# Performance work log

Hardware: AMD Instinct MI355X
Metric: run time of the kernel (lower is better)

## Reference

```python
import jax, jax.numpy as jnp
import numpy as np

K = 16        # neighbors
TAU = 0.1     # softmax temperature
BETA = 1.0    # knn loss weight
LAMB = 1e-4   # l2 reg weight
EPS = 1e-8    # clamp floor


def setup_inputs() -> dict:
    key = jax.random.key(0)
    k1, k2, k3, k4, k5, k6 = jax.random.split(key, 6)
    B, d, N, NQ = 256, 128, 100000, 4096
    q_batch = jax.random.normal(k1, (B, d), dtype=jnp.float32)
    q_indices = jax.random.randint(k2, (B,), 0, NQ, dtype=jnp.int64)
    X = jax.random.normal(k3, (N, d), dtype=jnp.float32)
    W = jax.random.normal(k4, (d, d), dtype=jnp.float32) * (1.0 / np.sqrt(d))
    pre_indices = jax.random.randint(k5, (NQ, K), 0, N, dtype=jnp.int64)
    pw = jax.random.uniform(k6, (NQ, K), dtype=jnp.float32) + 0.05
    pre_weights = pw / pw.sum(axis=1, keepdims=True)  # precomputed softmax weights
    return {"q_batch": q_batch, "q_indices": q_indices, "X": X, "W": W,
            "pre_indices": pre_indices, "pre_weights": pre_weights}


def reference(q_batch, q_indices, X, W, pre_indices, pre_weights):
    B = q_batch.shape[0]
    N = X.shape[0]
    # model(q_batch): linear map
    T_q = q_batch @ W  # [B, d]
    # brute-force faiss search: exact L2 top-K (indices are non-differentiable,
    # matching the detached faiss search in the original).
    Tq_sg = jax.lax.stop_gradient(T_q)
    d2 = (jnp.sum(Tq_sg * Tq_sg, axis=1, keepdims=True)
          + jnp.sum(X * X, axis=1)[None, :]
          - 2.0 * Tq_sg @ X.T)  # [B, N]
    _, post_idx = jax.lax.top_k(-d2, K)  # [B, K] nearest neighbors
    # recompute exact squared distances with gradient through T_q
    X_nb = X[post_idx]  # [B, K, d]
    l2 = jnp.sum((T_q[:, None, :] - X_nb) ** 2, axis=-1)  # [B, K]
    post_w = jax.nn.softmax(-l2 / TAU, axis=1)  # [B, K]
    # per-sample precomputed distributions
    pre_idx_b = pre_indices[q_indices]  # [B, K]
    pre_w_b = pre_weights[q_indices]    # [B, K]
    # dense scatter over the database axis (vectorized union construction)
    rows = jnp.arange(B)[:, None]
    p_dense = jnp.zeros((B, N), jnp.float32).at[rows, pre_idx_b].set(pre_w_b)
    q_dense = jnp.zeros((B, N), jnp.float32).at[rows, post_idx].set(post_w)
    union = (p_dense > 0) | (q_dense > 0)  # [B, N] union-of-indices mask
    p = jnp.where(union, jnp.maximum(p_dense, EPS), 0.0)
    p = p / p.sum(axis=1, keepdims=True)
    q = jnp.where(union, jnp.maximum(q_dense, EPS), 0.0)
    q = q / q.sum(axis=1, keepdims=True)
    # KL(p || q) summed over the union, averaged over batch
    logp = jnp.where(union, jnp.log(jnp.maximum(p, 1e-20)), 0.0)
    logq = jnp.where(union, jnp.log(jnp.maximum(q, 1e-20)), 0.0)
    kl = jnp.sum(jnp.where(union, p * (logp - logq), 0.0), axis=1)  # [B]
    loss_knn = jnp.mean(kl)
    loss_reg = 0.5 * jnp.sum(W * W)
    loss_dist = jnp.float32(0.0)
    total_loss = BETA * loss_knn + LAMB * loss_reg
    return (total_loss, loss_dist, loss_knn)
```

## Files before the change

### kernel.cpp

```cpp
#include <hip/hip_runtime.h>
#include <math.h>

#define KNN 16
#define DIM 128
#define BQ 256
#define NDB 100000
#define GRID 512
#define RPP 32
#define NCHUNK 3125
#define LONGB 53
#define XB_STR 136
#define MREG 8
#define CAPS 256
#define TAU_INV 10.0f
#define EPSC 1e-8f
#define FBIG 3.402823e38f

typedef float f32x4 __attribute__((ext_vector_type(4)));
typedef __bf16 bf16x8 __attribute__((ext_vector_type(8)));
typedef unsigned short ushort;
typedef ushort ushort8 __attribute__((ext_vector_type(8)));
typedef unsigned int uint4v __attribute__((ext_vector_type(4)));

__device__ __forceinline__ ushort f32_to_bf16_rne(float v) {
    unsigned bits = __float_as_uint(v);
    return (ushort)((bits + 0x7FFFu + ((bits >> 16) & 1u)) >> 16);
}
__device__ __forceinline__ unsigned pack2(float lo, float hi) {
    return (__float_as_uint(hi) & 0xFFFF0000u) | (__float_as_uint(lo) >> 16);
}
__device__ __forceinline__ float packv(float v, int id) {
    return __uint_as_float((__float_as_uint(v) & 0xFFFFFF00u) | (unsigned)id);
}

__global__ void k_tq(const float* __restrict__ qb, const float* __restrict__ W,
                     float* __restrict__ Tq, ushort* __restrict__ Tqb) {
    int b = blockIdx.x, c = threadIdx.x;
    __shared__ float qs[DIM];
    qs[c] = qb[b * DIM + c];
    __syncthreads();
    float acc = 0.f;
#pragma unroll 8
    for (int k = 0; k < DIM; ++k) acc = fmaf(qs[k], W[k * DIM + c], acc);
    Tq[b * DIM + c] = acc;
    Tqb[b * DIM + c] = f32_to_bf16_rne(acc);
}

__global__ __launch_bounds__(512, 2)
void k_pass0(const ushort* __restrict__ Tqb, const float* __restrict__ X,
             float* __restrict__ cand, float* __restrict__ blkmin_t) {
    __shared__ ushort xb[2][RPP * XB_STR];
    __shared__ float xsq_lds[2][RPP];
    const int t = threadIdx.x;
    const int w = t >> 6, lane = t & 63;
    const int la = lane >> 4, lb = lane & 15;
    const int sr = t >> 4, sc = t & 15;
    const int bid = blockIdx.x;
    const int nph = (bid < LONGB) ? 7 : 6;

    bf16x8 afr[2][4];
#pragma unroll
    for (int mt = 0; mt < 2; ++mt)
#pragma unroll
        for (int ks = 0; ks < 4; ++ks)
            afr[mt][ks] = *reinterpret_cast<const bf16x8*>(
                Tqb + (size_t)(w * 32 + mt * 16 + lb) * DIM + ks * 32 + la * 8);

    {
        const int rbase = bid * RPP;
        const float4* src = reinterpret_cast<const float4*>(X + (size_t)(rbase + sr) * DIM + sc * 8);
        float4 v0 = src[0], v1 = src[1];
        uint4v o = { pack2(v0.x, v0.y), pack2(v0.z, v0.w),
                     pack2(v1.x, v1.y), pack2(v1.z, v1.w) };
        *reinterpret_cast<uint4v*>(&xb[0][sr * XB_STR + sc * 8]) = o;
        float s = v0.x*v0.x + v0.y*v0.y + v0.z*v0.z + v0.w*v0.w
                + v1.x*v1.x + v1.y*v1.y + v1.z*v1.z + v1.w*v1.w;
        s += __shfl_xor(s, 1, 16); s += __shfl_xor(s, 2, 16);
        s += __shfl_xor(s, 4, 16); s += __shfl_xor(s, 8, 16);
        if (sc == 0) xsq_lds[0][sr] = s;
    }
    asm volatile("s_waitcnt lgkmcnt(0)" ::: "memory");
    __builtin_amdgcn_s_barrier();

    float t2_0[2][4], t2_1[2][4];
#pragma unroll
    for (int mt = 0; mt < 2; ++mt)
#pragma unroll
        for (int r = 0; r < 4; ++r) { t2_0[mt][r] = FBIG; t2_1[mt][r] = FBIG; }

#pragma unroll 1
    for (int p = 0; p < nph; ++p) {
        const int cur = p & 1, nxt = cur ^ 1;
        const int rb2 = (bid + ((p + 1) << 9)) << 5;
        float4 q0, q1;
        if (p + 1 < nph) {
            const float4* s2 = reinterpret_cast<const float4*>(X + (size_t)(rb2 + sr) * DIM + sc * 8);
            q0 = s2[0]; q1 = s2[1];
        }
#pragma unroll
        for (int nt = 0; nt < 2; ++nt) {
            const int row = nt * 16 + lb;
            bf16x8 bfr[4];
#pragma unroll
            for (int ks = 0; ks < 4; ++ks)
                bfr[ks] = *reinterpret_cast<const bf16x8*>(
                    &xb[cur][row * XB_STR + ks * 32 + la * 8]);
            const float xs = xsq_lds[cur][row];
            const int id = (((p << 1) | nt) << 4) | lb;
#pragma unroll
            for (int mt = 0; mt < 2; ++mt) {
                f32x4 acc = {0.f, 0.f, 0.f, 0.f};
#pragma unroll
                for (int ks = 0; ks < 4; ++ks)
                    acc = __builtin_amdgcn_mfma_f32_16x16x32_bf16(afr[mt][ks], bfr[ks], acc, 0, 0, 0);
#pragma unroll
                for (int r = 0; r < 4; ++r) {
                    float pv = packv(fmaf(-2.f, acc[r], xs), id);
                    float b0 = fminf(t2_0[mt][r], pv);
                    float hi = fmaxf(t2_0[mt][r], pv);
                    t2_1[mt][r] = fminf(t2_1[mt][r], hi);
                    t2_0[mt][r] = b0;
                }
            }
        }
        if (p + 1 < nph) {
            uint4v o = { pack2(q0.x, q0.y), pack2(q0.z, q0.w),
                         pack2(q1.x, q1.y), pack2(q1.z, q1.w) };
            *reinterpret_cast<uint4v*>(&xb[nxt][sr * XB_STR + sc * 8]) = o;
            float s = q0.x*q0.x + q0.y*q0.y + q0.z*q0.z + q0.w*q0.w
                    + q1.x*q1.x + q1.y*q1.y + q1.z*q1.z + q1.w*q1.w;
            s += __shfl_xor(s, 1, 16); s += __shfl_xor(s, 2, 16);
            s += __shfl_xor(s, 4, 16); s += __shfl_xor(s, 8, 16);
            if (sc == 0) xsq_lds[nxt][sr] = s;
            asm volatile("s_waitcnt lgkmcnt(0)" ::: "memory");
            __builtin_amdgcn_s_barrier();
        }
    }

#pragma unroll
    for (int mt = 0; mt < 2; ++mt)
#pragma unroll
        for (int r = 0; r < 4; ++r) {
            float a0 = t2_0[mt][r], a1 = t2_1[mt][r], a2 = FBIG, a3 = FBIG;
#pragma unroll
            for (int m = 1; m <= 8; m <<= 1) {
                float b0 = __shfl_xor(a0, m, 16), b1 = __shfl_xor(a1, m, 16);
                float b2 = __shfl_xor(a2, m, 16), b3 = __shfl_xor(a3, m, 16);
                float l0 = fminf(a0, b3), l1 = fminf(a1, b2);
                float l2 = fminf(a2, b1), l3 = fminf(a3, b0);
                float u;
                u = fminf(l0, l2); l2 = fmaxf(l0, l2); l0 = u;
                u = fminf(l1, l3); l3 = fmaxf(l1, l3); l1 = u;
                u = fminf(l0, l1); l1 = fmaxf(l0, l1); l0 = u;
                u = fminf(l2, l3); l3 = fmaxf(l2, l3); l2 = u;
                a0 = l0; a1 = l1; a2 = l2; a3 = l3;
            }
            if (lb == 0) {
                const int q = w * 32 + mt * 16 + la * 4 + r;
                f32x4 o4 = {a0, a1, a2, a3};
                *reinterpret_cast<f32x4*>(cand + (size_t)q * (GRID * 4) + bid * 4) = o4;
                blkmin_t[(size_t)q * GRID + bid] = a0;
            }
        }
}

__global__ __launch_bounds__(512)
void k_sel(const float* __restrict__ cand, const float* __restrict__ blkmin_t,
           const float* __restrict__ Tq, const float* __restrict__ X,
           const int* __restrict__ q_indices,
           const int* __restrict__ pre_indices,
           const float* __restrict__ pre_weights,
           float* __restrict__ klv) {
    const int q = blockIdx.x, t = threadIdx.x;
    __shared__ float tau_s;
    __shared__ int cnt_s;
    __shared__ float cv[CAPS]; __shared__ int ce[CAPS];
    __shared__ int post_idx[KNN];
    __shared__ float l2s[KNN];
    __shared__ float post_w[KNN];

    if (t == 0) cnt_s = 0;
    if (t < KNN) post_idx[t] = 0;
    if (t < 64) {
        float m[MREG];
#pragma unroll
        for (int k = 0; k < MREG; ++k)
            m[k] = blkmin_t[(size_t)q * GRID + t + (k << 6)];
        float tv = FBIG;
        for (int e = 0; e < KNN; ++e) {
            float best = m[0];
#pragma unroll
            for (int k = 1; k < MREG; ++k) best = fminf(best, m[k]);
            float b = best;
#pragma unroll
            for (int s = 1; s < 64; s <<= 1) b = fminf(b, __shfl_xor(b, s, 64));
            tv = b;
            unsigned long long has = __ballot(best == b);
            int src = (int)__builtin_ctzll(has);
            if (t == src) {
                bool dn = false;
#pragma unroll
                for (int k = 0; k < MREG; ++k) {
                    bool hit = !dn && (m[k] == b);
                    if (hit) { m[k] = FBIG; dn = true; }
                }
            }
        }
        if (t == 0) tau_s = tv;
    }
    __syncthreads();
    const float tau = tau_s;

    for (int e = t; e < GRID * 4; e += 512) {
        float pv = cand[(size_t)q * (GRID * 4) + e];
        if (pv <= tau) {
            int pos = atomicAdd(&cnt_s, 1);
            if (pos < CAPS) { cv[pos] = pv; ce[pos] = e; }
        }
    }
    __syncthreads();
    int n = cnt_s; n = (n > CAPS) ? CAPS : n;

    for (int e = t; e < n; e += 512) {
        float v = cv[e]; int id = ce[e];
        int r = 0;
        for (int i2 = 0; i2 < n; ++i2) {
            float vi = cv[i2];
            r += (vi < v) || (vi == v && ce[i2] < id);
        }
        if (r < KNN) {
            int bid = id >> 2;
            int sid = __float_as_uint(v) & 255;
            int j = (bid + (sid >> 5) * GRID) * RPP + ((sid >> 4) & 1) * 16 + (sid & 15);
            post_idx[r] = j;
        }
    }
    __syncthreads();

    if (t < 256) {
        int nn = t >> 4, l = t & 15;
        int idx = post_idx[nn];
        idx = (idx < 0) ? 0 : ((idx >= NDB) ? NDB - 1 : idx);
        const float* tr = Tq + q * DIM + l * 8;
        const float* xr = X + (size_t)idx * DIM + l * 8;
        float s = 0.f;
#pragma unroll
        for (int kk = 0; kk < 8; ++kk) { float df = tr[kk] - xr[kk]; s = fmaf(df, df, s); }
#pragma unroll
        for (int m = 1; m < 16; m <<= 1) s += __shfl_xor(s, m, 64);
        if (l == 0) l2s[nn] = s;
    }
    __syncthreads();

    if (t < 64) {
        float v = (t < KNN) ? (-l2s[t] * TAU_INV) : -FBIG;
        float mx = v;
#pragma unroll
        for (int m = 1; m < 16; m <<= 1) mx = fmaxf(mx, __shfl_xor(mx, m, 64));
        float e = (t < KNN) ? expf(v - mx) : 0.f;
        float sum = e;
#pragma unroll
        for (int m = 1; m < 16; m <<= 1) sum += __shfl_xor(sum, m, 64);
        if (t < KNN) post_w[t] = e / sum;

        int ui = (t < KNN) ? post_idx[t] : -1;
        float uq = (t < KNN) ? post_w[t] : 0.f;
        float up = 0.f;
        int cnt2 = KNN;
        const int qi = q_indices[q];
        for (int m = 0; m < KNN; ++m) {
            int pi = pre_indices[qi * KNN + m];
            float pwm = pre_weights[qi * KNN + m];
            unsigned long long mm = __ballot(ui == pi);
            if (mm) {
                if (t == (int)__builtin_ctzll(mm)) up = pwm;
            } else {
                if (t == cnt2) { ui = pi; up = pwm; uq = 0.f; }
                ++cnt2;
            }
        }
        float pe = 0.f, qe = 0.f, te = 0.f;
        if (t < cnt2) {
            pe = fmaxf(up, EPSC);
            qe = fmaxf(uq, EPSC);
            te = pe * (logf(pe) - logf(qe));
        }
        float Zp = pe, Zq = qe, T = te;
#pragma unroll
        for (int m = 1; m < 64; m <<= 1) {
            Zp += __shfl_xor(Zp, m, 64);
            Zq += __shfl_xor(Zq, m, 64);
            T  += __shfl_xor(T, m, 64);
        }
        if (t == 0) klv[q] = T / Zp - logf(Zp) + logf(Zq);
    }
}

__global__ void k_out(const float* __restrict__ kl, const float* __restrict__ W,
                      float* __restrict__ out) {
    int t = threadIdx.x;
    float s_kl = (t < BQ) ? kl[t] : 0.f;
    float s_w = 0.f;
    for (int i = t; i < DIM * DIM; i += 256) { float w = W[i]; s_w = fmaf(w, w, s_w); }
#pragma unroll
    for (int m = 32; m >= 1; m >>= 1) {
        s_kl += __shfl_xor(s_kl, m, 64);
        s_w += __shfl_xor(s_w, m, 64);
    }
    __shared__ float rk[4], rw[4];
    if ((t & 63) == 0) { rk[t >> 6] = s_kl; rw[t >> 6] = s_w; }
    __syncthreads();
    if (t == 0) {
        float kls = rk[0] + rk[1] + rk[2] + rk[3];
        float wss = rw[0] + rw[1] + rw[2] + rw[3];
        float knn = kls * (1.0f / BQ);
        float reg = 0.5f * wss;
        out[0] = 1.0f * knn + 1e-4f * reg;
        out[1] = 0.f;
        out[2] = knn;
    }
}

extern "C" void kernel_launch(void* const* d_in, const int* in_sizes, int n_in,
                              void* d_out, int out_size, void* d_ws, size_t ws_size,
                              hipStream_t stream) {
    const float* q_batch     = (const float*)d_in[0];
    const int*   q_indices   = (const int*)d_in[1];
    const float* X           = (const float*)d_in[2];
    const float* W           = (const float*)d_in[3];
    const int*   pre_indices = (const int*)d_in[4];
    const float* pre_weights = (const float*)d_in[5];

    char* ws = (char*)d_ws;
    float*  Tq      = (float*)(ws);
    ushort* Tqb     = (ushort*)(ws + 131072);
    float*  klv     = (float*)(ws + 196608);
    float*  blkmint = (float*)(ws + 262144);
    float*  cand    = (float*)(ws + 1048576);

    k_tq<<<dim3(BQ), dim3(DIM), 0, stream>>>(q_batch, W, Tq, Tqb);
    k_pass0<<<dim3(GRID), dim3(512), 0, stream>>>(Tqb, X, cand, blkmint);
    k_sel<<<dim3(BQ), dim3(512), 0, stream>>>(cand, blkmint, Tq, X,
                                              q_indices, pre_indices, pre_weights, klv);
    k_out<<<dim3(1), dim3(256), 0, stream>>>(klv, W, (float*)d_out);
}
```

Measured before the change: 63.43 us.

## Double rows per tile to 64 in the bf16 MFMA distance pass

Each block now stages 64 database rows per phase instead of 32, so there are half as many phases and barriers per block. Each thread loads 64 bytes per row chunk. Because 100000 is not a multiple of 64*512, the last chunk is padded: loads are clamped and out-of-range rows get distance FBIG. The packed candidate id encoding and its decode back to a database index are changed to match. The larger tile doubles LDS use, which may lower occupancy, and the final chunk partly wastes work.

```diff
diff --git a/kernel.cpp b/kernel.cpp
--- a/kernel.cpp
+++ b/kernel.cpp
@@ -6,9 +6,9 @@
 #define BQ 256
 #define NDB 100000
 #define GRID 512
-#define RPP 32
-#define NCHUNK 3125
-#define LONGB 53
+#define RPP 64
+#define NCHUNK 1563
+#define LONGB 27
 #define XB_STR 136
 #define MREG 8
 #define CAPS 256
@@ -19,7 +19,6 @@
 typedef float f32x4 __attribute__((ext_vector_type(4)));
 typedef __bf16 bf16x8 __attribute__((ext_vector_type(8)));
 typedef unsigned short ushort;
-typedef ushort ushort8 __attribute__((ext_vector_type(8)));
 typedef unsigned int uint4v __attribute__((ext_vector_type(4)));
 
 __device__ __forceinline__ ushort f32_to_bf16_rne(float v) {
@@ -54,9 +53,10 @@
     const int t = threadIdx.x;
     const int w = t >> 6, lane = t & 63;
     const int la = lane >> 4, lb = lane & 15;
-    const int sr = t >> 4, sc = t & 15;
+    const int sr = t >> 3;
+    const int sc = t & 7;
     const int bid = blockIdx.x;
-    const int nph = (bid < LONGB) ? 7 : 6;
+    const int nph = (bid < LONGB) ? 4 : 3;
 
     bf16x8 afr[2][4];
 #pragma unroll
@@ -67,16 +67,20 @@
                 Tqb + (size_t)(w * 32 + mt * 16 + lb) * DIM + ks * 32 + la * 8);
 
     {
-        const int rbase = bid * RPP;
-        const float4* src = reinterpret_cast<const float4*>(X + (size_t)(rbase + sr) * DIM + sc * 8);
-        float4 v0 = src[0], v1 = src[1];
-        uint4v o = { pack2(v0.x, v0.y), pack2(v0.z, v0.w),
-                     pack2(v1.x, v1.y), pack2(v1.z, v1.w) };
-        *reinterpret_cast<uint4v*>(&xb[0][sr * XB_STR + sc * 8]) = o;
+        int j = bid * RPP + sr; int jc = (j < NDB) ? j : (NDB - 1);
+        const float4* src = reinterpret_cast<const float4*>(X + (size_t)jc * DIM + sc * 16);
+        float4 v0 = src[0], v1 = src[1], v2 = src[2], v3 = src[3];
+        uint4v o0 = { pack2(v0.x, v0.y), pack2(v0.z, v0.w),
+                      pack2(v1.x, v1.y), pack2(v1.z, v1.w) };
+        uint4v o1 = { pack2(v2.x, v2.y), pack2(v2.z, v2.w),
+                      pack2(v3.x, v3.y), pack2(v3.z, v3.w) };
+        *reinterpret_cast<uint4v*>(&xb[0][sr * XB_STR + sc * 16]) = o0;
+        *reinterpret_cast<uint4v*>(&xb[0][sr * XB_STR + sc * 16 + 8]) = o1;
         float s = v0.x*v0.x + v0.y*v0.y + v0.z*v0.z + v0.w*v0.w
-                + v1.x*v1.x + v1.y*v1.y + v1.z*v1.z + v1.w*v1.w;
-        s += __shfl_xor(s, 1, 16); s += __shfl_xor(s, 2, 16);
-        s += __shfl_xor(s, 4, 16); s += __shfl_xor(s, 8, 16);
+                + v1.x*v1.x + v1.y*v1.y + v1.z*v1.z + v1.w*v1.w
+                + v2.x*v2.x + v2.y*v2.y + v2.z*v2.z + v2.w*v2.w
+                + v3.x*v3.x + v3.y*v3.y + v3.z*v3.z + v3.w*v3.w;
+        s += __shfl_xor(s, 1, 8); s += __shfl_xor(s, 2, 8); s += __shfl_xor(s, 4, 8);
         if (sc == 0) xsq_lds[0][sr] = s;
     }
     asm volatile("s_waitcnt lgkmcnt(0)" ::: "memory");
@@ -91,14 +95,16 @@
 #pragma unroll 1
     for (int p = 0; p < nph; ++p) {
         const int cur = p & 1, nxt = cur ^ 1;
-        const int rb2 = (bid + ((p + 1) << 9)) << 5;
-        float4 q0, q1;
+        const int cbase = (bid + ((p + 1) << 9)) * RPP;
+        float4 q0, q1, q2, q3;
         if (p + 1 < nph) {
-            const float4* s2 = reinterpret_cast<const float4*>(X + (size_t)(rb2 + sr) * DIM + sc * 8);
-            q0 = s2[0]; q1 = s2[1];
-        }
-#pragma unroll
-        for (int nt = 0; nt < 2; ++nt) {
+            int j = cbase + sr; int jc = (j < NDB) ? j : (NDB - 1);
+            const float4* s2 = reinterpret_cast<const float4*>(X + (size_t)jc * DIM + sc * 16);
+            q0 = s2[0]; q1 = s2[1]; q2 = s2[2]; q3 = s2[3];
+        }
+        const int rbase = (bid + (p << 9)) * RPP;
+#pragma unroll
+        for (int nt = 0; nt < 4; ++nt) {
             const int row = nt * 16 + lb;
             bf16x8 bfr[4];
 #pragma unroll
@@ -106,7 +112,9 @@
                 bfr[ks] = *reinterpret_cast<const bf16x8*>(
                     &xb[cur][row * XB_STR + ks * 32 + la * 8]);
             const float xs = xsq_lds[cur][row];
-            const int id = (((p << 1) | nt) << 4) | lb;
+            const int j = rbase + row;
+            const bool oob = (j >= NDB);
+            const int id = (((p << 2) | nt) << 4) | lb;
 #pragma unroll
             for (int mt = 0; mt < 2; ++mt) {
                 f32x4 acc = {0.f, 0.f, 0.f, 0.f};
@@ -115,7 +123,8 @@
                     acc = __builtin_amdgcn_mfma_f32_16x16x32_bf16(afr[mt][ks], bfr[ks], acc, 0, 0, 0);
 #pragma unroll
                 for (int r = 0; r < 4; ++r) {
-                    float pv = packv(fmaf(-2.f, acc[r], xs), id);
+                    float dv = oob ? FBIG : fmaf(-2.f, acc[r], xs);
+                    float pv = packv(dv, id);
                     float b0 = fminf(t2_0[mt][r], pv);
                     float hi = fmaxf(t2_0[mt][r], pv);
                     t2_1[mt][r] = fminf(t2_1[mt][r], hi);
@@ -124,13 +133,17 @@
             }
         }
         if (p + 1 < nph) {
-            uint4v o = { pack2(q0.x, q0.y), pack2(q0.z, q0.w),
-                         pack2(q1.x, q1.y), pack2(q1.z, q1.w) };
-            *reinterpret_cast<uint4v*>(&xb[nxt][sr * XB_STR + sc * 8]) = o;
+            uint4v o0 = { pack2(q0.x, q0.y), pack2(q0.z, q0.w),
+                          pack2(q1.x, q1.y), pack2(q1.z, q1.w) };
+            uint4v o1 = { pack2(q2.x, q2.y), pack2(q2.z, q2.w),
+                          pack2(q3.x, q3.y), pack2(q3.z, q3.w) };
+            *reinterpret_cast<uint4v*>(&xb[nxt][sr * XB_STR + sc * 16]) = o0;
+            *reinterpret_cast<uint4v*>(&xb[nxt][sr * XB_STR + sc * 16 + 8]) = o1;
             float s = q0.x*q0.x + q0.y*q0.y + q0.z*q0.z + q0.w*q0.w
-                    + q1.x*q1.x + q1.y*q1.y + q1.z*q1.z + q1.w*q1.w;
-            s += __shfl_xor(s, 1, 16); s += __shfl_xor(s, 2, 16);
-            s += __shfl_xor(s, 4, 16); s += __shfl_xor(s, 8, 16);
+                    + q1.x*q1.x + q1.y*q1.y + q1.z*q1.z + q1.w*q1.w
+                    + q2.x*q2.x + q2.y*q2.y + q2.z*q2.z + q2.w*q2.w
+                    + q3.x*q3.x + q3.y*q3.y + q3.z*q3.z + q3.w*q3.w;
+            s += __shfl_xor(s, 1, 8); s += __shfl_xor(s, 2, 8); s += __shfl_xor(s, 4, 8);
             if (sc == 0) xsq_lds[nxt][sr] = s;
             asm volatile("s_waitcnt lgkmcnt(0)" ::: "memory");
             __builtin_amdgcn_s_barrier();
@@ -231,7 +244,8 @@
         if (r < KNN) {
             int bid = id >> 2;
             int sid = __float_as_uint(v) & 255;
-            int j = (bid + (sid >> 5) * GRID) * RPP + ((sid >> 4) & 1) * 16 + (sid & 15);
+            int p2 = sid >> 6, nt = (sid >> 4) & 3, lb2 = sid & 15;
+            int j = (bid + (p2 << 9)) * RPP + nt * 16 + lb2;
             post_idx[r] = j;
         }
     }
```

Result: slower. 68.46 us (+7.9%).

## Deepen X prefetch to two phases and fold final reduction into atomics

Applied to the files above, without the earlier changes.

The distance pass now issues global loads for X tiles two phases ahead, holding them in registers, so each load has a full extra phase of MFMA work to cover its latency. The separate one-block output kernel is removed. The W squared-norm term is written by block 0 of the Tq kernel, and each selection block adds its scaled KL value to the output with atomics. This saves one kernel launch and its tail, at the cost of more live registers in the pass kernel and an output sum whose float rounding depends on atomic ordering.

```diff
diff --git a/kernel.cpp b/kernel.cpp
--- a/kernel.cpp
+++ b/kernel.cpp
@@ -19,7 +19,6 @@
 typedef float f32x4 __attribute__((ext_vector_type(4)));
 typedef __bf16 bf16x8 __attribute__((ext_vector_type(8)));
 typedef unsigned short ushort;
-typedef ushort ushort8 __attribute__((ext_vector_type(8)));
 typedef unsigned int uint4v __attribute__((ext_vector_type(4)));
 
 __device__ __forceinline__ ushort f32_to_bf16_rne(float v) {
@@ -34,7 +33,8 @@
 }
 
 __global__ void k_tq(const float* __restrict__ qb, const float* __restrict__ W,
-                     float* __restrict__ Tq, ushort* __restrict__ Tqb) {
+                     float* __restrict__ Tq, ushort* __restrict__ Tqb,
+                     float* __restrict__ out) {
     int b = blockIdx.x, c = threadIdx.x;
     __shared__ float qs[DIM];
     qs[c] = qb[b * DIM + c];
@@ -44,6 +44,21 @@
     for (int k = 0; k < DIM; ++k) acc = fmaf(qs[k], W[k * DIM + c], acc);
     Tq[b * DIM + c] = acc;
     Tqb[b * DIM + c] = f32_to_bf16_rne(acc);
+
+    if (b == 0) {
+        float sw = 0.f;
+        for (int i = c; i < DIM * DIM; i += 128) { float wv = W[i]; sw = fmaf(wv, wv, sw); }
+#pragma unroll
+        for (int m = 32; m >= 1; m >>= 1) sw += __shfl_xor(sw, m, 64);
+        __shared__ float rw2[2];
+        if ((c & 63) == 0) rw2[c >> 6] = sw;
+        __syncthreads();
+        if (c == 0) {
+            out[0] = 1e-4f * 0.5f * (rw2[0] + rw2[1]);
+            out[1] = 0.f;
+            out[2] = 0.f;
+        }
+    }
 }
 
 __global__ __launch_bounds__(512, 2)
@@ -66,6 +81,7 @@
             afr[mt][ks] = *reinterpret_cast<const bf16x8*>(
                 Tqb + (size_t)(w * 32 + mt * 16 + lb) * DIM + ks * 32 + la * 8);
 
+    float4 rA0, rA1;
     {
         const int rbase = bid * RPP;
         const float4* src = reinterpret_cast<const float4*>(X + (size_t)(rbase + sr) * DIM + sc * 8);
@@ -78,6 +94,11 @@
         s += __shfl_xor(s, 1, 16); s += __shfl_xor(s, 2, 16);
         s += __shfl_xor(s, 4, 16); s += __shfl_xor(s, 8, 16);
         if (sc == 0) xsq_lds[0][sr] = s;
+        if (nph > 1) {
+            const float4* s1 = reinterpret_cast<const float4*>(
+                X + (size_t)((bid + 512) * RPP + sr) * DIM + sc * 8);
+            rA0 = s1[0]; rA1 = s1[1];
+        }
     }
     asm volatile("s_waitcnt lgkmcnt(0)" ::: "memory");
     __builtin_amdgcn_s_barrier();
@@ -91,11 +112,11 @@
 #pragma unroll 1
     for (int p = 0; p < nph; ++p) {
         const int cur = p & 1, nxt = cur ^ 1;
-        const int rb2 = (bid + ((p + 1) << 9)) << 5;
-        float4 q0, q1;
-        if (p + 1 < nph) {
-            const float4* s2 = reinterpret_cast<const float4*>(X + (size_t)(rb2 + sr) * DIM + sc * 8);
-            q0 = s2[0]; q1 = s2[1];
+        float4 rB0, rB1;
+        if (p + 2 < nph) {
+            const float4* s2 = reinterpret_cast<const float4*>(
+                X + (size_t)((bid + ((p + 2) << 9)) * RPP + sr) * DIM + sc * 8);
+            rB0 = s2[0]; rB1 = s2[1];
         }
 #pragma unroll
         for (int nt = 0; nt < 2; ++nt) {
@@ -124,17 +145,18 @@
             }
         }
         if (p + 1 < nph) {
-            uint4v o = { pack2(q0.x, q0.y), pack2(q0.z, q0.w),
-                         pack2(q1.x, q1.y), pack2(q1.z, q1.w) };
+            uint4v o = { pack2(rA0.x, rA0.y), pack2(rA0.z, rA0.w),
+                         pack2(rA1.x, rA1.y), pack2(rA1.z, rA1.w) };
             *reinterpret_cast<uint4v*>(&xb[nxt][sr * XB_STR + sc * 8]) = o;
-            float s = q0.x*q0.x + q0.y*q0.y + q0.z*q0.z + q0.w*q0.w
-                    + q1.x*q1.x + q1.y*q1.y + q1.z*q1.z + q1.w*q1.w;
+            float s = rA0.x*rA0.x + rA0.y*rA0.y + rA0.z*rA0.z + rA0.w*rA0.w
+                    + rA1.x*rA1.x + rA1.y*rA1.y + rA1.z*rA1.z + rA1.w*rA1.w;
             s += __shfl_xor(s, 1, 16); s += __shfl_xor(s, 2, 16);
             s += __shfl_xor(s, 4, 16); s += __shfl_xor(s, 8, 16);
             if (sc == 0) xsq_lds[nxt][sr] = s;
             asm volatile("s_waitcnt lgkmcnt(0)" ::: "memory");
             __builtin_amdgcn_s_barrier();
         }
+        rA0 = rB0; rA1 = rB1;
     }
 
 #pragma unroll
@@ -170,7 +192,7 @@
            const int* __restrict__ q_indices,
            const int* __restrict__ pre_indices,
            const float* __restrict__ pre_weights,
-           float* __restrict__ klv) {
+           float* __restrict__ out) {
     const int q = blockIdx.x, t = threadIdx.x;
     __shared__ float tau_s;
     __shared__ int cnt_s;
@@ -292,32 +314,11 @@
             Zq += __shfl_xor(Zq, m, 64);
             T  += __shfl_xor(T, m, 64);
         }
-        if (t == 0) klv[q] = T / Zp - logf(Zp) + logf(Zq);
-    }
-}
-
-__global__ void k_out(const float* __restrict__ kl, const float* __restrict__ W,
-                      float* __restrict__ out) {
-    int t = threadIdx.x;
-    float s_kl = (t < BQ) ? kl[t] : 0.f;
-    float s_w = 0.f;
-    for (int i = t; i < DIM * DIM; i += 256) { float w = W[i]; s_w = fmaf(w, w, s_w); }
-#pragma unroll
-    for (int m = 32; m >= 1; m >>= 1) {
-        s_kl += __shfl_xor(s_kl, m, 64);
-        s_w += __shfl_xor(s_w, m, 64);
-    }
-    __shared__ float rk[4], rw[4];
-    if ((t & 63) == 0) { rk[t >> 6] = s_kl; rw[t >> 6] = s_w; }
-    __syncthreads();
-    if (t == 0) {
-        float kls = rk[0] + rk[1] + rk[2] + rk[3];
-        float wss = rw[0] + rw[1] + rw[2] + rw[3];
-        float knn = kls * (1.0f / BQ);
-        float reg = 0.5f * wss;
-        out[0] = 1.0f * knn + 1e-4f * reg;
-        out[1] = 0.f;
-        out[2] = knn;
+        if (t == 0) {
+            float kl = (T / Zp - logf(Zp) + logf(Zq)) * (1.0f / BQ);
+            atomicAdd(out + 0, kl);
+            atomicAdd(out + 2, kl);
+        }
     }
 }
 
@@ -334,13 +335,12 @@
     char* ws = (char*)d_ws;
     float*  Tq      = (float*)(ws);
     ushort* Tqb     = (ushort*)(ws + 131072);
-    float*  klv     = (float*)(ws + 196608);
     float*  blkmint = (float*)(ws + 262144);
     float*  cand    = (float*)(ws + 1048576);
-
-    k_tq<<<dim3(BQ), dim3(DIM), 0, stream>>>(q_batch, W, Tq, Tqb);
+    float*  outp    = (float*)d_out;
+
+    k_tq<<<dim3(BQ), dim3(DIM), 0, stream>>>(q_batch, W, Tq, Tqb, outp);
     k_pass0<<<dim3(GRID), dim3(512), 0, stream>>>(Tqb, X, cand, blkmint);
     k_sel<<<dim3(BQ), dim3(512), 0, stream>>>(cand, blkmint, Tq, X,
-                                              q_indices, pre_indices, pre_weights, klv);
-    k_out<<<dim3(1), dim3(256), 0, stream>>>(klv, W, (float*)d_out);
-}
+                                              q_indices, pre_indices, pre_weights, outp);
+}
```

Result: no change. 64.45 us (+1.6%).
